# Optimization experiments

Hardware: AMD Instinct MI355X
Metric: run time of the kernel (lower is better)

## Reference

```python
import jax, jax.numpy as jnp
import numpy as np
import math

B, T, C = 4, 2048, 1024
NH = 16
HD = C // NH


def setup_inputs() -> dict:
    key = jax.random.key(0)
    ks = jax.random.split(key, 10)
    s = 0.02
    x = jax.random.normal(ks[0], (B, T, C), dtype=jnp.float32)
    W_qkv = jax.random.normal(ks[1], (C, 3 * C), dtype=jnp.float32) * s
    b_qkv = jnp.zeros((3 * C,), dtype=jnp.float32)
    W_proj = jax.random.normal(ks[2], (C, C), dtype=jnp.float32) * s
    b_proj = jnp.zeros((C,), dtype=jnp.float32)
    asym_mean, asym_std = 1.0, 0.7
    q_scale = jax.random.normal(ks[3], (NH, HD), dtype=jnp.float32) * asym_std + asym_mean
    q_bias = jax.random.normal(ks[4], (NH, HD), dtype=jnp.float32) * asym_std + asym_mean
    k_scale = jax.random.normal(ks[5], (NH, HD), dtype=jnp.float32) * asym_std + asym_mean
    k_bias = jax.random.normal(ks[6], (NH, HD), dtype=jnp.float32) * asym_std + asym_mean
    return {"x": x, "W_qkv": W_qkv, "b_qkv": b_qkv, "W_proj": W_proj,
            "b_proj": b_proj, "q_scale": q_scale, "q_bias": q_bias,
            "k_scale": k_scale, "k_bias": k_bias}


def reference(x, W_qkv, b_qkv, W_proj, b_proj, q_scale, q_bias, k_scale, k_bias):
    Bx, Tx, Cx = x.shape
    qkv = x @ W_qkv + b_qkv                       # [B,T,3C]
    q, k, v = jnp.split(qkv, 3, axis=-1)
    # [B,T,C] -> [B,NH,T,HD]
    reshape = lambda t: t.reshape(Bx, Tx, NH, HD).transpose(0, 2, 1, 3)
    q, k, v = reshape(q), reshape(k), reshape(v)
    # per-head affine scaling of Q/K
    q = q * q_scale[None, :, None, :] + q_bias[None, :, None, :]
    k = k * k_scale[None, :, None, :] + k_bias[None, :, None, :]
    scores = jnp.einsum('bhqd,bhkd->bhqk', q, k) / math.sqrt(HD)  # [B,NH,T,T]
    causal = jnp.tril(jnp.ones((Tx, Tx), dtype=bool))
    scores = jnp.where(causal[None, None], scores, -jnp.inf)
    att = jax.nn.softmax(scores, axis=-1)
    y = jnp.einsum('bhqk,bhkd->bhqd', att, v)     # [B,NH,T,HD]
    y = y.transpose(0, 2, 1, 3).reshape(Bx, Tx, Cx)
    return y @ W_proj + b_proj
```

## Files before the change

kernel.cpp:

```cpp
#include <hip/hip_runtime.h>
#include <hip/hip_bf16.h>

typedef unsigned short u16;
typedef __attribute__((ext_vector_type(8))) short short8;
typedef __attribute__((ext_vector_type(4))) float floatx4;

#define B_SZ 4
#define T_SZ 2048
#define C_SZ 1024
#define NH_SZ 16
#define HD_SZ 64
#define M_TOT 8192
#define K_DIM 1024

#define QSCALE 0.1803368801111204f

#define OFF_XB   ((size_t)16)
#define OFF_WQT  (OFF_XB + 8388608)
#define OFF_WPT  (OFF_WQT + 3145728)
#define OFF_PB   (OFF_WPT + 1048576)
#define OFF_Q    (OFF_PB + 8192)
#define OFF_K    (OFF_Q + 8388608)
#define OFF_V    (OFF_K + 8388608)
#define OFF_Y    (OFF_V + 8388608)
#define PB_BQKV  0
#define PB_BPROJ 3072
#define PB_QSC   4096
#define PB_QBI   5120
#define PB_KSC   6144
#define PB_KBI   7168

__device__ __forceinline__ float bf2f(u16 u) {
    return __uint_as_float(((unsigned)u) << 16);
}
__device__ __forceinline__ u16 f2bf(float f) {
    unsigned x = __float_as_uint(f);
    unsigned r = (x + 0x7fffu + ((x >> 16) & 1u)) >> 16;
    return (u16)r;
}
__device__ __forceinline__ void gl_lds16(const u16* g, u16* l) {
    __builtin_amdgcn_global_load_lds(
        (const __attribute__((address_space(1))) void*)g,
        (__attribute__((address_space(3))) void*)l, 16, 0, 0);
}

__global__ __launch_bounds__(256) void detect_k(const u16* __restrict__ x,
                                                int* __restrict__ flag) {
    __shared__ int cnt;
    if (threadIdx.x == 0) cnt = 0;
    __syncthreads();
    int bad = 0;
    for (int i = threadIdx.x; i < 512; i += 256) {
        float v = fabsf(bf2f(x[i]));
        if (v > 1024.0f || (v != 0.0f && v < 9.5367431640625e-7f)) bad++;
    }
    atomicAdd(&cnt, bad);
    __syncthreads();
    if (threadIdx.x == 0) flag[0] = (cnt > 16) ? 1 : 0;
}

__global__ __launch_bounds__(256) void conv_copy_k(const void* __restrict__ in,
                                                   u16* __restrict__ out, int n4,
                                                   const int* __restrict__ flag) {
    const int i = blockIdx.x * 256 + threadIdx.x;
    if (i >= n4) return;
    if (flag[0]) {
        const float4 v = ((const float4*)in)[i];
        ushort4 o;
        o.x = f2bf(v.x); o.y = f2bf(v.y); o.z = f2bf(v.z); o.w = f2bf(v.w);
        ((ushort4*)out)[i] = o;
    } else {
        ((ushort4*)out)[i] = ((const ushort4*)in)[i];
    }
}

__global__ __launch_bounds__(256) void conv_params_k(
        const void* __restrict__ bqkv, const void* __restrict__ bproj,
        const void* __restrict__ qsc, const void* __restrict__ qbi,
        const void* __restrict__ ksc, const void* __restrict__ kbi,
        u16* __restrict__ pb, const int* __restrict__ flag) {
    const int i4 = blockIdx.x * 256 + threadIdx.x;
    if (i4 >= 2048) return;
    const int e = i4 * 4;
    const void* src; int off;
    if (e < 3072)      { src = bqkv;  off = e; }
    else if (e < 4096) { src = bproj; off = e - 3072; }
    else if (e < 5120) { src = qsc;   off = e - 4096; }
    else if (e < 6144) { src = qbi;   off = e - 5120; }
    else if (e < 7168) { src = ksc;   off = e - 6144; }
    else               { src = kbi;   off = e - 7168; }
    ushort4 o;
    if (flag[0]) {
        const float4 v = *(const float4*)((const float*)src + off);
        o.x = f2bf(v.x); o.y = f2bf(v.y); o.z = f2bf(v.z); o.w = f2bf(v.w);
    } else {
        o = *(const ushort4*)((const u16*)src + off);
    }
    *(ushort4*)&pb[e] = o;
}

__global__ __launch_bounds__(256) void conv_transpose_k(const void* __restrict__ in,
                                                        u16* __restrict__ out,
                                                        int R, int C,
                                                        const int* __restrict__ flag) {
    __shared__ u16 t[32][33];
    const int isf = flag[0];
    const int c0 = blockIdx.x * 32, r0 = blockIdx.y * 32;
    const int tx = threadIdx.x & 31, ty = threadIdx.x >> 5;
    for (int i = 0; i < 4; i++) {
        int r = ty + i * 8;
        size_t idx = (size_t)(r0 + r) * C + c0 + tx;
        t[r][tx] = isf ? f2bf(((const float*)in)[idx]) : ((const u16*)in)[idx];
    }
    __syncthreads();
    for (int i = 0; i < 4; i++) {
        int cr = ty + i * 8;
        out[(size_t)(c0 + cr) * R + r0 + tx] = t[tx][cr];
    }
}

__global__ __launch_bounds__(256) void qkv_gemm(
        const u16* __restrict__ X, const u16* __restrict__ Wt,
        const u16* __restrict__ pb,
        u16* __restrict__ Qb, u16* __restrict__ Kb, u16* __restrict__ Vb) {
    __shared__ __align__(16) u16 As[128 * 64];
    __shared__ __align__(16) u16 Bs[128 * 64];
    const int bm = blockIdx.y * 128, bn = blockIdx.x * 128;
    const int tid = threadIdx.x;
    const int lane = tid & 63, wave = tid >> 6;
    const int quad = lane >> 4, l16 = lane & 15;
    const int wm = (wave & 1) * 64, wn = (wave >> 1) * 64;
    const int lrow = lane >> 3;
    const int lcol = ((lane & 7) ^ lrow) * 8;

    floatx4 acc[4][4];
    for (int mi = 0; mi < 4; mi++)
        for (int ni = 0; ni < 4; ni++) acc[mi][ni] = 0.f;

    for (int k0 = 0; k0 < K_DIM; k0 += 64) {
        __syncthreads();
        for (int j = 0; j < 4; j++) {
            const int rb = wave * 32 + j * 8;
            gl_lds16(&X[(size_t)(bm + rb + lrow) * K_DIM + k0 + lcol], &As[rb * 64]);
            gl_lds16(&Wt[(size_t)(bn + rb + lrow) * K_DIM + k0 + lcol], &Bs[rb * 64]);
        }
        __syncthreads();
        for (int kk = 0; kk < 64; kk += 32) {
            const int cb = kk >> 3;
            const int slot = ((cb + quad) ^ (l16 & 7)) * 8;
            short8 a[4], b[4];
            for (int mi = 0; mi < 4; mi++)
                a[mi] = *(const short8*)&As[(wm + mi * 16 + l16) * 64 + slot];
            for (int ni = 0; ni < 4; ni++)
                b[ni] = *(const short8*)&Bs[(wn + ni * 16 + l16) * 64 + slot];
            for (int mi = 0; mi < 4; mi++)
                for (int ni = 0; ni < 4; ni++)
                    acc[mi][ni] = __builtin_amdgcn_mfma_f32_16x16x32_bf16(
                        a[mi], b[ni], acc[mi][ni], 0, 0, 0);
        }
    }

    const int sec = bn >> 10;
    const int bb = bm >> 11;
    const int tbase = bm & 2047;
    for (int mi = 0; mi < 4; mi++) {
        for (int ni = 0; ni < 4; ni++) {
            const int col = bn + wn + ni * 16 + l16;
            const int cmod = col & 1023;
            const int h = cmod >> 6, d = cmod & 63;
            const float bv = bf2f(pb[PB_BQKV + col]);
            if (sec == 2) {
                const int t0 = tbase + wm + mi * 16 + quad * 4;
                ushort4 pk;
                pk.x = f2bf(acc[mi][ni][0] + bv);
                pk.y = f2bf(acc[mi][ni][1] + bv);
                pk.z = f2bf(acc[mi][ni][2] + bv);
                pk.w = f2bf(acc[mi][ni][3] + bv);
                *(ushort4*)&Vb[(((size_t)(bb * NH_SZ + h)) * HD_SZ + d) * T_SZ + t0] = pk;
            } else {
                float sA, sB;
                if (sec == 0) {
                    sA = bf2f(pb[PB_QSC + h * 64 + d]) * QSCALE;
                    sB = bf2f(pb[PB_QBI + h * 64 + d]) * QSCALE;
                } else {
                    sA = bf2f(pb[PB_KSC + h * 64 + d]);
                    sB = bf2f(pb[PB_KBI + h * 64 + d]);
                }
                u16* dstbuf = (sec == 0) ? Qb : Kb;
                for (int r = 0; r < 4; r++) {
                    const int t = tbase + wm + mi * 16 + quad * 4 + r;
                    float v = (acc[mi][ni][r] + bv) * sA + sB;
                    dstbuf[(((size_t)(bb * NH_SZ + h)) * T_SZ + t) * HD_SZ + d] = f2bf(v);
                }
            }
        }
    }
}

__global__ __launch_bounds__(512) void attn_k(const u16* __restrict__ Qb,
                                              const u16* __restrict__ Kb,
                                              const u16* __restrict__ Vtg,
                                              u16* __restrict__ Y) {
    __shared__ __align__(16) u16 Ks[64 * 72];
    __shared__ __align__(16) u16 Vs[64 * 72];
    __shared__ __align__(16) u16 Ps[8 * 16 * 88];
    const int blk = blockIdx.x;
    const int head = blk & 63;
    const int p = blk >> 6;
    const int b = head >> 4, h = head & 15;
    const int tid = threadIdx.x, lane = tid & 63, w = tid >> 6;
    const int quad = lane >> 4, l16 = lane & 15;
    const size_t qk_off = (size_t)head * (T_SZ * HD_SZ);
    const size_t v_off = (size_t)head * (HD_SZ * T_SZ);
    u16* psw = &Ps[w * 1408];

    for (int tile = 0; tile < 2; tile++) {
        const int qt = tile ? p : (15 - p);
        const int q0 = qt * 128;
        const int rbase = q0 + w * 16;
        const int q = rbase + l16;

        const short8 aq0 = *(const short8*)&Qb[qk_off + (size_t)q * HD_SZ + quad * 8];
        const short8 aq1 = *(const short8*)&Qb[qk_off + (size_t)q * HD_SZ + 32 + quad * 8];

        floatx4 o[4];
        for (int mi = 0; mi < 4; mi++) o[mi] = 0.f;
        float m_run = -1e30f, l_run = 0.f;

        for (int k0 = 0; k0 < q0 + 128; k0 += 64) {
            __syncthreads();
            {
                int r = tid >> 3, c8 = (tid & 7) * 8;
                *(float4*)&Ks[r * 72 + c8] =
                    *(const float4*)&Kb[qk_off + (size_t)(k0 + r) * HD_SZ + c8];
                *(float4*)&Vs[r * 72 + c8] =
                    *(const float4*)&Vtg[v_off + (size_t)r * T_SZ + k0 + c8];
            }
            __syncthreads();
            if (k0 > rbase + 15) continue;

            floatx4 s[4];
            for (int ni = 0; ni < 4; ni++) s[ni] = 0.f;
            for (int ni = 0; ni < 4; ni++)
                s[ni] = __builtin_amdgcn_mfma_f32_16x16x32_bf16(
                    *(const short8*)&Ks[(ni * 16 + l16) * 72 + quad * 8], aq0, s[ni], 0, 0, 0);
            for (int ni = 0; ni < 4; ni++)
                s[ni] = __builtin_amdgcn_mfma_f32_16x16x32_bf16(
                    *(const short8*)&Ks[(ni * 16 + l16) * 72 + 32 + quad * 8], aq1, s[ni], 0, 0, 0);

            if (k0 + 63 > rbase) {
                for (int ni = 0; ni < 4; ni++)
                    for (int r = 0; r < 4; r++) {
                        int key = k0 + ni * 16 + quad * 4 + r;
                        if (key > q) s[ni][r] = -1e30f;
                    }
            }

            float mx = s[0][0];
            for (int ni = 0; ni < 4; ni++)
                for (int r = 0; r < 4; r++) mx = fmaxf(mx, s[ni][r]);
            mx = fmaxf(mx, __shfl_xor(mx, 16, 64));
            mx = fmaxf(mx, __shfl_xor(mx, 32, 64));
            const float mnew = fmaxf(m_run, mx);
            const float alpha = exp2f(m_run - mnew);
            float rsum = 0.f;
            for (int ni = 0; ni < 4; ni++)
                for (int r = 0; r < 4; r++) {
                    float pv = exp2f(s[ni][r] - mnew);
                    s[ni][r] = pv;
                    rsum += pv;
                }
            rsum += __shfl_xor(rsum, 16, 64);
            rsum += __shfl_xor(rsum, 32, 64);
            m_run = mnew;
            l_run = l_run * alpha + rsum;
            for (int mi = 0; mi < 4; mi++) o[mi] *= alpha;

            for (int ni = 0; ni < 4; ni++) {
                ushort4 pk;
                pk.x = f2bf(s[ni][0]); pk.y = f2bf(s[ni][1]);
                pk.z = f2bf(s[ni][2]); pk.w = f2bf(s[ni][3]);
                *(ushort4*)&psw[l16 * 88 + ni * 16 + quad * 4] = pk;
            }

            for (int kk = 0; kk < 64; kk += 32) {
                short8 pfr = *(const short8*)&psw[l16 * 88 + kk + quad * 8];
                for (int mi = 0; mi < 4; mi++) {
                    short8 vfr = *(const short8*)&Vs[(mi * 16 + l16) * 72 + kk + quad * 8];
                    o[mi] = __builtin_amdgcn_mfma_f32_16x16x32_bf16(vfr, pfr, o[mi], 0, 0, 0);
                }
            }
        }

        const float inv = 1.0f / l_run;
        u16* yrow = &Y[(((size_t)b * T_SZ + q) * NH_SZ + h) * HD_SZ];
        for (int mi = 0; mi < 4; mi++) {
            ushort4 pk;
            pk.x = f2bf(o[mi][0] * inv); pk.y = f2bf(o[mi][1] * inv);
            pk.z = f2bf(o[mi][2] * inv); pk.w = f2bf(o[mi][3] * inv);
            *(ushort4*)&yrow[mi * 16 + quad * 4] = pk;
        }
    }
}

__global__ __launch_bounds__(256) void proj_gemm(const u16* __restrict__ Yin,
                                                 const u16* __restrict__ Wt,
                                                 const u16* __restrict__ pb,
                                                 void* __restrict__ out,
                                                 const int* __restrict__ flag) {
    __shared__ __align__(16) u16 As[128 * 64];
    __shared__ __align__(16) u16 Bs[128 * 64];
    const int isf = flag[0];
    const int bm = blockIdx.y * 128, bn = blockIdx.x * 128;
    const int tid = threadIdx.x;
    const int lane = tid & 63, wave = tid >> 6;
    const int quad = lane >> 4, l16 = lane & 15;
    const int wm = (wave & 1) * 64, wn = (wave >> 1) * 64;
    const int lrow = lane >> 3;
    const int lcol = ((lane & 7) ^ lrow) * 8;

    floatx4 acc[4][4];
    for (int mi = 0; mi < 4; mi++)
        for (int ni = 0; ni < 4; ni++) acc[mi][ni] = 0.f;

    for (int k0 = 0; k0 < K_DIM; k0 += 64) {
        __syncthreads();
        for (int j = 0; j < 4; j++) {
            const int rb = wave * 32 + j * 8;
            gl_lds16(&Yin[(size_t)(bm + rb + lrow) * K_DIM + k0 + lcol], &As[rb * 64]);
            gl_lds16(&Wt[(size_t)(bn + rb + lrow) * K_DIM + k0 + lcol], &Bs[rb * 64]);
        }
        __syncthreads();
        for (int kk = 0; kk < 64; kk += 32) {
            const int cb = kk >> 3;
            const int slot = ((cb + quad) ^ (l16 & 7)) * 8;
            short8 a[4], b[4];
            for (int mi = 0; mi < 4; mi++)
                a[mi] = *(const short8*)&As[(wm + mi * 16 + l16) * 64 + slot];
            for (int ni = 0; ni < 4; ni++)
                b[ni] = *(const short8*)&Bs[(wn + ni * 16 + l16) * 64 + slot];
            for (int mi = 0; mi < 4; mi++)
                for (int ni = 0; ni < 4; ni++)
                    acc[mi][ni] = __builtin_amdgcn_mfma_f32_16x16x32_bf16(
                        a[mi], b[ni], acc[mi][ni], 0, 0, 0);
        }
    }

    for (int mi = 0; mi < 4; mi++) {
        for (int ni = 0; ni < 4; ni++) {
            const int col = bn + wn + ni * 16 + l16;
            const float bv = bf2f(pb[PB_BPROJ + col]);
            for (int r = 0; r < 4; r++) {
                const int row = bm + wm + mi * 16 + quad * 4 + r;
                const float v = acc[mi][ni][r] + bv;
                if (isf) ((float*)out)[(size_t)row * C_SZ + col] = v;
                else     ((u16*)out)[(size_t)row * C_SZ + col] = f2bf(v);
            }
        }
    }
}

extern "C" void kernel_launch(void* const* d_in, const int* in_sizes, int n_in,
                              void* d_out, int out_size, void* d_ws, size_t ws_size,
                              hipStream_t stream) {
    const void* x     = d_in[0];
    const void* Wqkv  = d_in[1];
    const void* bqkv  = d_in[2];
    const void* Wproj = d_in[3];
    const void* bproj = d_in[4];
    const void* qsc   = d_in[5];
    const void* qbi   = d_in[6];
    const void* ksc   = d_in[7];
    const void* kbi   = d_in[8];

    u16* ws = (u16*)d_ws;
    int* flag    = (int*)d_ws;
    u16* xb      = ws + OFF_XB;
    u16* Wt_qkv  = ws + OFF_WQT;
    u16* Wt_proj = ws + OFF_WPT;
    u16* pb      = ws + OFF_PB;
    u16* Qb      = ws + OFF_Q;
    u16* Kb      = ws + OFF_K;
    u16* Vb      = ws + OFF_V;
    u16* Yb      = ws + OFF_Y;

    detect_k<<<1, 256, 0, stream>>>((const u16*)x, flag);

    conv_copy_k<<<8192, 256, 0, stream>>>(x, xb, 2097152, flag);
    conv_params_k<<<8, 256, 0, stream>>>(bqkv, bproj, qsc, qbi, ksc, kbi, pb, flag);
    conv_transpose_k<<<dim3(96, 32), 256, 0, stream>>>(Wqkv, Wt_qkv, 1024, 3072, flag);
    conv_transpose_k<<<dim3(32, 32), 256, 0, stream>>>(Wproj, Wt_proj, 1024, 1024, flag);

    qkv_gemm<<<dim3(24, 64), 256, 0, stream>>>(xb, Wt_qkv, pb, Qb, Kb, Vb);
    attn_k<<<dim3(512), 512, 0, stream>>>(Qb, Kb, Vb, Yb);
    proj_gemm<<<dim3(8, 64), 256, 0, stream>>>(Yb, Wt_proj, pb, d_out, flag);
}
```

Baseline: 323.5 us.

## Use direct global-to-LDS loads with XOR swizzle and MFMA row sums in attention

```diff
diff --git a/kernel.cpp b/kernel.cpp
--- a/kernel.cpp
+++ b/kernel.cpp
@@ -37,6 +37,9 @@
     unsigned x = __float_as_uint(f);
     unsigned r = (x + 0x7fffu + ((x >> 16) & 1u)) >> 16;
     return (u16)r;
+}
+__device__ __forceinline__ u16 f2bf_fast(float f) {
+    return (u16)((__float_as_uint(f) + 0x8000u) >> 16);
 }
 __device__ __forceinline__ void gl_lds16(const u16* g, u16* l) {
     __builtin_amdgcn_global_load_lds(
@@ -201,8 +204,8 @@
                                               const u16* __restrict__ Kb,
                                               const u16* __restrict__ Vtg,
                                               u16* __restrict__ Y) {
-    __shared__ __align__(16) u16 Ks[64 * 72];
-    __shared__ __align__(16) u16 Vs[64 * 72];
+    __shared__ __align__(16) u16 Ks[64 * 64];
+    __shared__ __align__(16) u16 Vs[64 * 64];
     __shared__ __align__(16) u16 Ps[8 * 16 * 88];
     const int blk = blockIdx.x;
     const int head = blk & 63;
@@ -213,6 +216,13 @@
     const size_t qk_off = (size_t)head * (T_SZ * HD_SZ);
     const size_t v_off = (size_t)head * (HD_SZ * T_SZ);
     u16* psw = &Ps[w * 1408];
+    const int lr = lane >> 3;
+    const int lc = ((lane & 7) ^ lr) * 8;
+    const int sl0 = ((quad) ^ (l16 & 7)) * 8;
+    const int sl1 = ((4 + quad) ^ (l16 & 7)) * 8;
+
+    short8 ones;
+    for (int j = 0; j < 8; j++) ones[j] = (short)0x3F80;
 
     for (int tile = 0; tile < 2; tile++) {
         const int qt = tile ? p : (15 - p);
@@ -229,13 +239,8 @@
 
         for (int k0 = 0; k0 < q0 + 128; k0 += 64) {
             __syncthreads();
-            {
-                int r = tid >> 3, c8 = (tid & 7) * 8;
-                *(float4*)&Ks[r * 72 + c8] =
-                    *(const float4*)&Kb[qk_off + (size_t)(k0 + r) * HD_SZ + c8];
-                *(float4*)&Vs[r * 72 + c8] =
-                    *(const float4*)&Vtg[v_off + (size_t)r * T_SZ + k0 + c8];
-            }
+            gl_lds16(&Kb[qk_off + (size_t)(k0 + w * 8 + lr) * HD_SZ + lc], &Ks[w * 512]);
+            gl_lds16(&Vtg[v_off + (size_t)(w * 8 + lr) * T_SZ + k0 + lc], &Vs[w * 512]);
             __syncthreads();
             if (k0 > rbase + 15) continue;
 
@@ -243,10 +248,10 @@
             for (int ni = 0; ni < 4; ni++) s[ni] = 0.f;
             for (int ni = 0; ni < 4; ni++)
                 s[ni] = __builtin_amdgcn_mfma_f32_16x16x32_bf16(
-                    *(const short8*)&Ks[(ni * 16 + l16) * 72 + quad * 8], aq0, s[ni], 0, 0, 0);
+                    *(const short8*)&Ks[(ni * 16 + l16) * 64 + sl0], aq0, s[ni], 0, 0, 0);
             for (int ni = 0; ni < 4; ni++)
                 s[ni] = __builtin_amdgcn_mfma_f32_16x16x32_bf16(
-                    *(const short8*)&Ks[(ni * 16 + l16) * 72 + 32 + quad * 8], aq1, s[ni], 0, 0, 0);
+                    *(const short8*)&Ks[(ni * 16 + l16) * 64 + sl1], aq1, s[ni], 0, 0, 0);
 
             if (k0 + 63 > rbase) {
                 for (int ni = 0; ni < 4; ni++)
@@ -256,48 +261,48 @@
                     }
             }
 
-            float mx = s[0][0];
-            for (int ni = 0; ni < 4; ni++)
-                for (int r = 0; r < 4; r++) mx = fmaxf(mx, s[ni][r]);
+            float mx = fmaxf(fmaxf(s[0][0], s[0][1]), fmaxf(s[0][2], s[0][3]));
+            for (int ni = 1; ni < 4; ni++)
+                mx = fmaxf(mx, fmaxf(fmaxf(s[ni][0], s[ni][1]),
+                                     fmaxf(s[ni][2], s[ni][3])));
             mx = fmaxf(mx, __shfl_xor(mx, 16, 64));
             mx = fmaxf(mx, __shfl_xor(mx, 32, 64));
             const float mnew = fmaxf(m_run, mx);
             const float alpha = exp2f(m_run - mnew);
-            float rsum = 0.f;
             for (int ni = 0; ni < 4; ni++)
-                for (int r = 0; r < 4; r++) {
-                    float pv = exp2f(s[ni][r] - mnew);
-                    s[ni][r] = pv;
-                    rsum += pv;
-                }
-            rsum += __shfl_xor(rsum, 16, 64);
-            rsum += __shfl_xor(rsum, 32, 64);
+                for (int r = 0; r < 4; r++)
+                    s[ni][r] = exp2f(s[ni][r] - mnew);
             m_run = mnew;
-            l_run = l_run * alpha + rsum;
             for (int mi = 0; mi < 4; mi++) o[mi] *= alpha;
 
             for (int ni = 0; ni < 4; ni++) {
                 ushort4 pk;
-                pk.x = f2bf(s[ni][0]); pk.y = f2bf(s[ni][1]);
-                pk.z = f2bf(s[ni][2]); pk.w = f2bf(s[ni][3]);
+                pk.x = f2bf_fast(s[ni][0]); pk.y = f2bf_fast(s[ni][1]);
+                pk.z = f2bf_fast(s[ni][2]); pk.w = f2bf_fast(s[ni][3]);
                 *(ushort4*)&psw[l16 * 88 + ni * 16 + quad * 4] = pk;
             }
 
+            floatx4 s4 = 0.f;
             for (int kk = 0; kk < 64; kk += 32) {
+                const int sl = (kk == 0) ? 0 : 0;
                 short8 pfr = *(const short8*)&psw[l16 * 88 + kk + quad * 8];
+                const int vsl = (kk == 0) ? sl0 : sl1;
+                s4 = __builtin_amdgcn_mfma_f32_16x16x32_bf16(ones, pfr, s4, 0, 0, 0);
                 for (int mi = 0; mi < 4; mi++) {
-                    short8 vfr = *(const short8*)&Vs[(mi * 16 + l16) * 72 + kk + quad * 8];
+                    short8 vfr = *(const short8*)&Vs[(mi * 16 + l16) * 64 + vsl];
                     o[mi] = __builtin_amdgcn_mfma_f32_16x16x32_bf16(vfr, pfr, o[mi], 0, 0, 0);
                 }
+                (void)sl;
             }
+            l_run = l_run * alpha + s4[0];
         }
 
         const float inv = 1.0f / l_run;
         u16* yrow = &Y[(((size_t)b * T_SZ + q) * NH_SZ + h) * HD_SZ];
         for (int mi = 0; mi < 4; mi++) {
             ushort4 pk;
-            pk.x = f2bf(o[mi][0] * inv); pk.y = f2bf(o[mi][1] * inv);
-            pk.z = f2bf(o[mi][2] * inv); pk.w = f2bf(o[mi][3] * inv);
+            pk.x = f2bf_fast(o[mi][0] * inv); pk.y = f2bf_fast(o[mi][1] * inv);
+            pk.z = f2bf_fast(o[mi][2] * inv); pk.w = f2bf_fast(o[mi][3] * inv);
             *(ushort4*)&yrow[mi * 16 + quad * 4] = pk;
         }
     }
```

Result: faster. 317.0 us (-2.0%).
